# Performance work log

Hardware: AMD Instinct MI355X
Metric: run time of the kernel (lower is better)

Reference implementation:

```python
import jax, jax.numpy as jnp
import numpy as np

D_MODEL = 512
N_HEADS = 8
HEAD_SIZE = 64


def setup_inputs() -> dict:
    key = jax.random.key(0)
    ks = jax.random.split(key, 6)
    B, T = 4, 2048
    x_q = jax.random.normal(ks[0], (B, T, D_MODEL), dtype=jnp.float32)
    s = 1.0 / np.sqrt(D_MODEL)
    # per-head q/k/v projection weights, stacked: [H, head_size, d_model]
    Wq = jax.random.normal(ks[1], (N_HEADS, HEAD_SIZE, D_MODEL), dtype=jnp.float32) * s
    Wk = jax.random.normal(ks[2], (N_HEADS, HEAD_SIZE, D_MODEL), dtype=jnp.float32) * s
    Wv = jax.random.normal(ks[3], (N_HEADS, HEAD_SIZE, D_MODEL), dtype=jnp.float32) * s
    Wp = jax.random.normal(ks[4], (D_MODEL, D_MODEL), dtype=jnp.float32) * s
    bp = jax.random.normal(ks[5], (D_MODEL,), dtype=jnp.float32) * 0.01
    return {"x_q": x_q, "Wq": Wq, "Wk": Wk, "Wv": Wv, "Wp": Wp, "bp": bp}


def reference(x_q, Wq, Wk, Wv, Wp, bp):
    B, T, C = x_q.shape  # C == d_model
    # per-head projections: [B, H, T, K]
    q = jnp.einsum('btd,hkd->bhtk', x_q, Wq)
    k = jnp.einsum('btd,hkd->bhtk', x_q, Wk)
    v = jnp.einsum('btd,hkd->bhtk', x_q, Wv)
    # NOTE: original scales by C**-0.5 with C = d_model (not head_size)
    scores = jnp.einsum('bhtk,bhsk->bhts', q, k) * (C ** -0.5)
    causal = jnp.tril(jnp.ones((T, T), dtype=bool))
    scores = jnp.where(causal, scores, -jnp.inf)
    wei = jax.nn.softmax(scores, axis=-1)  # dropout is identity in eval
    out = jnp.einsum('bhts,bhsk->bhtk', wei, v)
    # concat heads: [B, T, H*K] == [B, T, d_model]
    out = out.transpose(0, 2, 1, 3).reshape(B, T, C)
    return out @ Wp.T + bp
```

## Files before the change

### kernel.cpp

```cpp
#include <hip/hip_runtime.h>
#include <hip/hip_bf16.h>

using bf16x8 = __attribute__((ext_vector_type(8))) __bf16;
using f32x4  = __attribute__((ext_vector_type(4))) float;
using f32x16 = __attribute__((ext_vector_type(16))) float;
using i32x4  = __attribute__((ext_vector_type(4))) int;

#define MFMA_16x16x32(a, b, c) __builtin_amdgcn_mfma_f32_16x16x32_bf16((a), (b), (c), 0, 0, 0)
#define MFMA32(a, b, c)        __builtin_amdgcn_mfma_f32_32x32x16_bf16((a), (b), (c), 0, 0, 0)

__device__ __forceinline__ ushort f2bf(float f) {
    return __builtin_bit_cast(ushort, (__bf16)f);
}
__device__ __forceinline__ unsigned pk_bf16(float lo, float hi) {
    unsigned r;
    asm volatile("v_cvt_pk_bf16_f32 %0, %1, %2" : "=v"(r) : "v"(lo), "v"(hi));
    return r;
}
__device__ __forceinline__ void pl32_swap(unsigned &a, unsigned &b) {
    asm volatile("v_permlane32_swap_b32 %0, %1" : "+v"(a), "+v"(b));
}

__global__ __launch_bounds__(256) void cvt_bf16(
    const float* __restrict__ in, ushort* __restrict__ out, int n)
{
    const int i = (blockIdx.x * 256 + threadIdx.x) * 8;
    if (i + 8 <= n) {
        const f32x4 a = *(const f32x4*)(in + i);
        const f32x4 b = *(const f32x4*)(in + i + 4);
        union { ushort u[8]; i32x4 w; } p;
        #pragma unroll
        for (int j = 0; j < 4; ++j) { p.u[j] = f2bf(a[j]); p.u[4 + j] = f2bf(b[j]); }
        *(i32x4*)(out + i) = p.w;
    }
}

__global__ __launch_bounds__(256) void gemm_qkv3(
    const ushort* __restrict__ A, const float* __restrict__ Wq,
    const float* __restrict__ Wk, const float* __restrict__ Wv,
    float qscale, ushort* __restrict__ qb, ushort* __restrict__ kb,
    ushort* __restrict__ vb)
{
    __shared__ ushort lA[128][40];
    __shared__ ushort lB[128][40];
    const int wsel = blockIdx.y >> 2;
    const int n0 = (blockIdx.y & 3) * 128;
    const float* W = (wsel == 0) ? Wq : ((wsel == 1) ? Wk : Wv);
    ushort* out = (wsel == 0) ? qb : ((wsel == 1) ? kb : vb);
    const float scale = (wsel == 0) ? qscale : 1.0f;

    const int m0 = blockIdx.x * 128;
    const int tid  = threadIdx.x;
    const int lane = tid & 63;
    const int wave = tid >> 6;
    const int wr = (wave >> 1) * 64, wc = (wave & 1) * 64;
    const int frow = lane & 15, fk = (lane >> 4) * 8;
    const int sr = tid >> 1, scc = (tid & 1) * 16;

    f32x4 acc[4][4] = {};

    for (int k0 = 0; k0 < 512; k0 += 32) {
        const ushort* pa = A + (m0 + sr) * 512 + k0 + scc;
        const i32x4 va0 = *(const i32x4*)(pa);
        const i32x4 va1 = *(const i32x4*)(pa + 8);
        const float* pb = W + (n0 + sr) * 512 + k0 + scc;
        const f32x4 b0 = *(const f32x4*)(pb);
        const f32x4 b1 = *(const f32x4*)(pb + 4);
        const f32x4 b2 = *(const f32x4*)(pb + 8);
        const f32x4 b3 = *(const f32x4*)(pb + 12);
        union { ushort u[16]; i32x4 w[2]; } pB;
        #pragma unroll
        for (int j = 0; j < 4; ++j) {
            pB.u[j]      = f2bf(b0[j]);  pB.u[4 + j]  = f2bf(b1[j]);
            pB.u[8 + j]  = f2bf(b2[j]);  pB.u[12 + j] = f2bf(b3[j]);
        }
        __syncthreads();
        *(i32x4*)&lA[sr][scc]     = va0;
        *(i32x4*)&lA[sr][scc + 8] = va1;
        *(i32x4*)&lB[sr][scc]     = pB.w[0];
        *(i32x4*)&lB[sr][scc + 8] = pB.w[1];
        __syncthreads();

        bf16x8 af[4], bg[4];
        #pragma unroll
        for (int m = 0; m < 4; ++m) af[m] = *(const bf16x8*)&lA[wr + m * 16 + frow][fk];
        #pragma unroll
        for (int n = 0; n < 4; ++n) bg[n] = *(const bf16x8*)&lB[wc + n * 16 + frow][fk];
        #pragma unroll
        for (int m = 0; m < 4; ++m)
            #pragma unroll
            for (int n = 0; n < 4; ++n)
                acc[m][n] = MFMA_16x16x32(af[m], bg[n], acc[m][n]);
    }

    const int rbase = (lane >> 4) * 4;
    const int ccol  = lane & 15;
    if (wsel == 2) {
        #pragma unroll
        for (int m = 0; m < 4; ++m)
            #pragma unroll
            for (int n = 0; n < 4; ++n) {
                const int col = n0 + wc + n * 16 + ccol;
                const int row0 = m0 + wr + m * 16 + rbase;
                unsigned long long u = 0;
                #pragma unroll
                for (int r = 0; r < 4; ++r)
                    u |= ((unsigned long long)f2bf(acc[m][n][r])) << (16 * r);
                const size_t idx = ((size_t)((row0 >> 11) * 8 + (col >> 6)) * 64
                                    + (col & 63)) * 2048 + (row0 & 2047);
                *(unsigned long long*)(out + idx) = u;
            }
    } else {
        #pragma unroll
        for (int m = 0; m < 4; ++m)
            #pragma unroll
            for (int n = 0; n < 4; ++n) {
                const int col = n0 + wc + n * 16 + ccol;
                #pragma unroll
                for (int r = 0; r < 4; ++r) {
                    const int row = m0 + wr + m * 16 + rbase + r;
                    out[(((row >> 11) * 8 + (col >> 6)) * 2048 + (row & 2047)) * 64 + (col & 63)]
                        = f2bf(acc[m][n][r] * scale);
                }
            }
    }
}

__global__ __launch_bounds__(256) void gemm_out(
    const ushort* __restrict__ A, const float* __restrict__ W,
    const float* __restrict__ bias, float* __restrict__ out)
{
    __shared__ ushort lA[128][40];
    __shared__ ushort lB[128][40];
    const int m0 = blockIdx.x * 128;
    const int n0 = blockIdx.y * 128;
    const int tid  = threadIdx.x;
    const int lane = tid & 63;
    const int wave = tid >> 6;
    const int wr = (wave >> 1) * 64, wc = (wave & 1) * 64;
    const int frow = lane & 15, fk = (lane >> 4) * 8;
    const int sr = tid >> 1, scc = (tid & 1) * 16;

    f32x4 acc[4][4] = {};

    for (int k0 = 0; k0 < 512; k0 += 32) {
        const int row = m0 + sr, c = k0 + scc;
        const ushort* pa = A + ((((row >> 11) * 8 + (c >> 6)) * 2048 + (row & 2047)) * 64 + (c & 63));
        const i32x4 va0 = *(const i32x4*)(pa);
        const i32x4 va1 = *(const i32x4*)(pa + 8);
        const float* pb = W + (n0 + sr) * 512 + k0 + scc;
        const f32x4 b0 = *(const f32x4*)(pb);
        const f32x4 b1 = *(const f32x4*)(pb + 4);
        const f32x4 b2 = *(const f32x4*)(pb + 8);
        const f32x4 b3 = *(const f32x4*)(pb + 12);
        union { ushort u[16]; i32x4 w[2]; } pB;
        #pragma unroll
        for (int j = 0; j < 4; ++j) {
            pB.u[j]      = f2bf(b0[j]);  pB.u[4 + j]  = f2bf(b1[j]);
            pB.u[8 + j]  = f2bf(b2[j]);  pB.u[12 + j] = f2bf(b3[j]);
        }
        __syncthreads();
        *(i32x4*)&lA[sr][scc]     = va0;
        *(i32x4*)&lA[sr][scc + 8] = va1;
        *(i32x4*)&lB[sr][scc]     = pB.w[0];
        *(i32x4*)&lB[sr][scc + 8] = pB.w[1];
        __syncthreads();

        bf16x8 af[4], bg[4];
        #pragma unroll
        for (int m = 0; m < 4; ++m) af[m] = *(const bf16x8*)&lA[wr + m * 16 + frow][fk];
        #pragma unroll
        for (int n = 0; n < 4; ++n) bg[n] = *(const bf16x8*)&lB[wc + n * 16 + frow][fk];
        #pragma unroll
        for (int m = 0; m < 4; ++m)
            #pragma unroll
            for (int n = 0; n < 4; ++n)
                acc[m][n] = MFMA_16x16x32(af[m], bg[n], acc[m][n]);
    }

    const int rbase = (lane >> 4) * 4;
    const int ccol  = lane & 15;
    #pragma unroll
    for (int m = 0; m < 4; ++m)
        #pragma unroll
        for (int n = 0; n < 4; ++n) {
            const int col = n0 + wc + n * 16 + ccol;
            const float bv = bias[col];
            #pragma unroll
            for (int r = 0; r < 4; ++r) {
                const int row = m0 + wr + m * 16 + rbase + r;
                out[row * 512 + col] = acc[m][n][r] + bv;
            }
        }
}

__global__ __launch_bounds__(256, 2) void attn_kernel(
    const ushort* __restrict__ q, const ushort* __restrict__ k,
    const ushort* __restrict__ vt, ushort* __restrict__ att)
{
    __shared__ ushort lK[2][64][64];
    __shared__ ushort lV[2][64][64];

    const int NB   = (int)(gridDim.x * gridDim.y);
    const int NH   = NB >> 4;
    const int half = NB >> 1;
    const int n    = (int)(blockIdx.y * gridDim.x + blockIdx.x);
    const int r    = (n < half) ? n : (NB - 1 - (n - half));
    const int qt0  = (15 - r / NH) * 128;
    const int bh   = r % NH;

    const ushort* Q  = q  + (size_t)bh * 2048 * 64;
    const ushort* K  = k  + (size_t)bh * 2048 * 64;
    const ushort* VT = vt + (size_t)bh * 2048 * 64;
    ushort* O = att + (size_t)bh * 2048 * 64;

    const int tid = threadIdx.x;
    const int wv  = tid >> 6;
    const int l   = tid & 63;
    const int ql  = l & 31;
    const int hi  = l >> 5;
    const int wrow0 = qt0 + wv * 32;
    const int qrow  = wrow0 + ql;
    const int wmax  = wrow0 + 31;
    const int qkey  = ql & 7;
    const float LOG2E = 1.44269504088896f;

    const int srow = tid >> 2;
    const int sg   = (tid & 3) * 2;
    const int skey = srow & 7;

    bf16x8 aq[4];
    #pragma unroll
    for (int kk = 0; kk < 4; ++kk)
        aq[kk] = *(const bf16x8*)(Q + (size_t)qrow * 64 + kk * 16 + hi * 8);

    f32x16 o0 = {}, o1 = {};
    float mrun = -30000.0f, lrun = 0.0f;
    const int nt = qt0 / 64 + 2;

    i32x4 kr0, kr1, vr0, vr1;
    auto loadG = [&](int s0) {
        const ushort* kp = K + (size_t)(s0 + srow) * 64 + (tid & 3) * 16;
        kr0 = *(const i32x4*)(kp);
        kr1 = *(const i32x4*)(kp + 8);
        const ushort* vp = VT + (size_t)srow * 2048 + s0 + (tid & 3) * 16;
        vr0 = *(const i32x4*)(vp);
        vr1 = *(const i32x4*)(vp + 8);
    };
    auto writeL = [&](int b) {
        *(i32x4*)&lK[b][srow][((sg    ) ^ skey) * 8] = kr0;
        *(i32x4*)&lK[b][srow][((sg + 1) ^ skey) * 8] = kr1;
        *(i32x4*)&lV[b][srow][((sg    ) ^ skey) * 8] = vr0;
        *(i32x4*)&lV[b][srow][((sg + 1) ^ skey) * 8] = vr1;
    };

    loadG(0);
    writeL(0);
    if (nt > 1) loadG(64);

    for (int t = 0; t < nt; ++t) {
        const int p  = t & 1;
        const int s0 = t * 64;
        __syncthreads();
        if (t + 1 < nt) writeL(p ^ 1);
        if (t + 2 < nt) loadG(s0 + 128);

        if (s0 > wmax) continue;

        f32x16 sa = {}, sb = {};
        #pragma unroll
        for (int kk = 0; kk < 4; ++kk) {
            const bf16x8 kb0 = *(const bf16x8*)&lK[p][ql]     [((2 * kk + hi) ^ qkey) * 8];
            const bf16x8 kb1 = *(const bf16x8*)&lK[p][32 + ql][((2 * kk + hi) ^ qkey) * 8];
            sa = MFMA32(kb0, aq[kk], sa);
            sb = MFMA32(kb1, aq[kk], sb);
        }

        if (s0 + 63 > wrow0) {
            #pragma unroll
            for (int rr = 0; rr < 16; ++rr) {
                const int cr = (rr & 3) + 8 * (rr >> 2) + 4 * hi;
                if (s0 + cr > qrow)      sa[rr] = -30000.0f;
                if (s0 + 32 + cr > qrow) sb[rr] = -30000.0f;
            }
        }

        float pmax = sa[0];
        #pragma unroll
        for (int rr = 1; rr < 16; ++rr) pmax = fmaxf(pmax, sa[rr]);
        #pragma unroll
        for (int rr = 0; rr < 16; ++rr) pmax = fmaxf(pmax, sb[rr]);
        pmax = fmaxf(pmax, __shfl_xor(pmax, 32));

        if (__any(pmax > mrun + 8.0f)) {
            const float mnew  = fmaxf(mrun, pmax);
            const float alpha = exp2f((mrun - mnew) * LOG2E);
            mrun = mnew;
            lrun *= alpha;
            #pragma unroll
            for (int rr = 0; rr < 16; ++rr) {
                const float ar = __shfl(alpha, (rr & 3) + 8 * (rr >> 2) + 4 * hi);
                o0[rr] *= ar; o1[rr] *= ar;
            }
        }

        const float mb = mrun * LOG2E;
        float ps = 0.0f;
        #pragma unroll
        for (int rr = 0; rr < 16; ++rr) {
            sa[rr] = exp2f(fmaf(sa[rr], LOG2E, -mb));
            sb[rr] = exp2f(fmaf(sb[rr], LOG2E, -mb));
            ps += sa[rr] + sb[rr];
        }
        ps += __shfl_xor(ps, 32);
        lrun += ps;

        unsigned paw[4][4];
        #pragma unroll
        for (int ks = 0; ks < 4; ++ks) {
            const int e = 2 * ks, f = 2 * ks + 1;
            const int ra = 4 * (e & 3), rb = 4 * (f & 3);
            unsigned A0, A1, B0, B1;
            if (e >> 2) { A0 = pk_bf16(sb[ra], sb[ra + 1]); A1 = pk_bf16(sb[ra + 2], sb[ra + 3]); }
            else        { A0 = pk_bf16(sa[ra], sa[ra + 1]); A1 = pk_bf16(sa[ra + 2], sa[ra + 3]); }
            if (f >> 2) { B0 = pk_bf16(sb[rb], sb[rb + 1]); B1 = pk_bf16(sb[rb + 2], sb[rb + 3]); }
            else        { B0 = pk_bf16(sa[rb], sa[rb + 1]); B1 = pk_bf16(sa[rb + 2], sa[rb + 3]); }
            pl32_swap(A0, B0);
            pl32_swap(A1, B1);
            paw[ks][0] = A0; paw[ks][1] = A1; paw[ks][2] = B0; paw[ks][3] = B1;
        }

        #pragma unroll
        for (int ks = 0; ks < 4; ++ks) {
            union { unsigned w[4]; bf16x8 v; } u;
            u.w[0] = paw[ks][0]; u.w[1] = paw[ks][1];
            u.w[2] = paw[ks][2]; u.w[3] = paw[ks][3];
            const bf16x8 v0 = *(const bf16x8*)&lV[p][ql]     [((2 * ks + hi) ^ qkey) * 8];
            const bf16x8 v1 = *(const bf16x8*)&lV[p][32 + ql][((2 * ks + hi) ^ qkey) * 8];
            o0 = MFMA32(u.v, v0, o0);
            o1 = MFMA32(u.v, v1, o1);
        }
    }

    const float linv = 1.0f / fmaxf(lrun, 1e-30f);
    #pragma unroll
    for (int rr = 0; rr < 16; ++rr) {
        const int cr = (rr & 3) + 8 * (rr >> 2) + 4 * hi;
        const float li = __shfl(linv, cr);
        const int row = wrow0 + cr;
        O[(size_t)row * 64 + ql]      = f2bf(o0[rr] * li);
        O[(size_t)row * 64 + 32 + ql] = f2bf(o1[rr] * li);
    }
}

extern "C" void kernel_launch(void* const* d_in, const int* in_sizes, int n_in,
                              void* d_out, int out_size, void* d_ws, size_t ws_size,
                              hipStream_t stream) {
    const float* x  = (const float*)d_in[0];
    const float* Wq = (const float*)d_in[1];
    const float* Wk = (const float*)d_in[2];
    const float* Wv = (const float*)d_in[3];
    const float* Wp = (const float*)d_in[4];
    const float* bp = (const float*)d_in[5];
    float* out = (float*)d_out;

    const size_t NEL  = 4u * 8u * 2048u * 64u;
    const size_t NELB = 8u * 2048u * 64u;
    const float qscale = 0.04419417382415922f;

    if (ws_size >= 3u * NEL * sizeof(ushort)) {
        ushort* xbf = (ushort*)d_out;
        ushort* qb  = xbf + NEL;
        ushort* kb  = (ushort*)d_ws;
        ushort* vb  = kb + NEL;
        ushort* ab  = vb + NEL;
        hipLaunchKernelGGL(cvt_bf16, dim3((int)(NEL / (256 * 8))), dim3(256), 0, stream,
                           x, xbf, (int)NEL);
        hipLaunchKernelGGL(gemm_qkv3, dim3(64, 12), dim3(256), 0, stream,
                           xbf, Wq, Wk, Wv, qscale, qb, kb, vb);
        hipLaunchKernelGGL(attn_kernel, dim3(16, 32), dim3(256), 0, stream, qb, kb, vb, ab);
        hipLaunchKernelGGL(gemm_out, dim3(64, 4), dim3(256), 0, stream, ab, Wp, bp, out);
    } else {
        ushort* kb = (ushort*)d_ws;
        ushort* vb = kb + NELB;
        ushort* ab = vb + NELB;
        for (int b = 0; b < 4; ++b) {
            const float* xb = x + (size_t)b * 2048u * 512u;
            float* ob = out + (size_t)b * 2048u * 512u;
            ushort* xbf = (ushort*)ob;
            ushort* qb  = xbf + NELB;
            hipLaunchKernelGGL(cvt_bf16, dim3((int)(NELB / (256 * 8))), dim3(256), 0, stream,
                               xb, xbf, (int)NELB);
            hipLaunchKernelGGL(gemm_qkv3, dim3(16, 12), dim3(256), 0, stream,
                               xbf, Wq, Wk, Wv, qscale, qb, kb, vb);
            hipLaunchKernelGGL(attn_kernel, dim3(16, 8), dim3(256), 0, stream, qb, kb, vb, ab);
            hipLaunchKernelGGL(gemm_out, dim3(16, 4), dim3(256), 0, stream, ab, Wp, bp, ob);
        }
    }
}
```

Baseline: 109.9 us.

## Pre-convert QKV weights to bf16 and halve attention query tile to 64 rows

Adds a kernel that converts Wq/Wk/Wv to bf16 once into the workspace (reusing the attention output buffer), so the QKV GEMM loads bf16 weights directly instead of converting fp32 in every tile. The attention kernel moves from 256 threads and 128-row query tiles to 128 threads and 64-row tiles, doubling the grid. The K/V staging is re-indexed so each thread loads four 16-byte chunks. This aims for more blocks and better causal load balance, at the cost of one extra launch and more K/V tile reloads per query row.

Result: slower. 119.8 us (+9.0%).

```diff
diff --git a/kernel.cpp b/kernel.cpp
--- a/kernel.cpp
+++ b/kernel.cpp
@@ -35,9 +35,23 @@
     }
 }
 
+__global__ __launch_bounds__(256) void cvt_w3(
+    const float* __restrict__ w0, const float* __restrict__ w1,
+    const float* __restrict__ w2, ushort* __restrict__ out)
+{
+    const int i = (blockIdx.x * 256 + threadIdx.x) * 8;
+    const int w = i >> 18, off = i & 262143;
+    const float* src = (w == 0) ? w0 : ((w == 1) ? w1 : w2);
+    const f32x4 a = *(const f32x4*)(src + off);
+    const f32x4 b = *(const f32x4*)(src + off + 4);
+    union { ushort u[8]; i32x4 v; } p;
+    #pragma unroll
+    for (int j = 0; j < 4; ++j) { p.u[j] = f2bf(a[j]); p.u[4 + j] = f2bf(b[j]); }
+    *(i32x4*)(out + i) = p.v;
+}
+
 __global__ __launch_bounds__(256) void gemm_qkv3(
-    const ushort* __restrict__ A, const float* __restrict__ Wq,
-    const float* __restrict__ Wk, const float* __restrict__ Wv,
+    const ushort* __restrict__ A, const ushort* __restrict__ Wbf,
     float qscale, ushort* __restrict__ qb, ushort* __restrict__ kb,
     ushort* __restrict__ vb)
 {
@@ -45,7 +59,7 @@
     __shared__ ushort lB[128][40];
     const int wsel = blockIdx.y >> 2;
     const int n0 = (blockIdx.y & 3) * 128;
-    const float* W = (wsel == 0) ? Wq : ((wsel == 1) ? Wk : Wv);
+    const ushort* W = Wbf + wsel * 262144;
     ushort* out = (wsel == 0) ? qb : ((wsel == 1) ? kb : vb);
     const float scale = (wsel == 0) ? qscale : 1.0f;
 
@@ -63,22 +77,14 @@
         const ushort* pa = A + (m0 + sr) * 512 + k0 + scc;
         const i32x4 va0 = *(const i32x4*)(pa);
         const i32x4 va1 = *(const i32x4*)(pa + 8);
-        const float* pb = W + (n0 + sr) * 512 + k0 + scc;
-        const f32x4 b0 = *(const f32x4*)(pb);
-        const f32x4 b1 = *(const f32x4*)(pb + 4);
-        const f32x4 b2 = *(const f32x4*)(pb + 8);
-        const f32x4 b3 = *(const f32x4*)(pb + 12);
-        union { ushort u[16]; i32x4 w[2]; } pB;
-        #pragma unroll
-        for (int j = 0; j < 4; ++j) {
-            pB.u[j]      = f2bf(b0[j]);  pB.u[4 + j]  = f2bf(b1[j]);
-            pB.u[8 + j]  = f2bf(b2[j]);  pB.u[12 + j] = f2bf(b3[j]);
-        }
+        const ushort* pb = W + (n0 + sr) * 512 + k0 + scc;
+        const i32x4 vb0 = *(const i32x4*)(pb);
+        const i32x4 vb1 = *(const i32x4*)(pb + 8);
         __syncthreads();
         *(i32x4*)&lA[sr][scc]     = va0;
         *(i32x4*)&lA[sr][scc + 8] = va1;
-        *(i32x4*)&lB[sr][scc]     = pB.w[0];
-        *(i32x4*)&lB[sr][scc + 8] = pB.w[1];
+        *(i32x4*)&lB[sr][scc]     = vb0;
+        *(i32x4*)&lB[sr][scc + 8] = vb1;
         __syncthreads();
 
         bf16x8 af[4], bg[4];
@@ -194,7 +200,7 @@
         }
 }
 
-__global__ __launch_bounds__(256, 2) void attn_kernel(
+__global__ __launch_bounds__(128) void attn_kernel(
     const ushort* __restrict__ q, const ushort* __restrict__ k,
     const ushort* __restrict__ vt, ushort* __restrict__ att)
 {
@@ -202,11 +208,11 @@
     __shared__ ushort lV[2][64][64];
 
     const int NB   = (int)(gridDim.x * gridDim.y);
-    const int NH   = NB >> 4;
+    const int NH   = (int)gridDim.y;
     const int half = NB >> 1;
     const int n    = (int)(blockIdx.y * gridDim.x + blockIdx.x);
     const int r    = (n < half) ? n : (NB - 1 - (n - half));
-    const int qt0  = (15 - r / NH) * 128;
+    const int qt0  = ((int)gridDim.x - 1 - r / NH) * 64;
     const int bh   = r % NH;
 
     const ushort* Q  = q  + (size_t)bh * 2048 * 64;
@@ -225,8 +231,8 @@
     const int qkey  = ql & 7;
     const float LOG2E = 1.44269504088896f;
 
-    const int srow = tid >> 2;
-    const int sg   = (tid & 3) * 2;
+    const int srow = tid >> 1;
+    const int sg   = (tid & 1) * 4;
     const int skey = srow & 7;
 
     bf16x8 aq[4];
@@ -236,22 +242,24 @@
 
     f32x16 o0 = {}, o1 = {};
     float mrun = -30000.0f, lrun = 0.0f;
-    const int nt = qt0 / 64 + 2;
-
-    i32x4 kr0, kr1, vr0, vr1;
+    const int nt = qt0 / 64 + 1;
+
+    i32x4 kr[4], vr[4];
     auto loadG = [&](int s0) {
-        const ushort* kp = K + (size_t)(s0 + srow) * 64 + (tid & 3) * 16;
-        kr0 = *(const i32x4*)(kp);
-        kr1 = *(const i32x4*)(kp + 8);
-        const ushort* vp = VT + (size_t)srow * 2048 + s0 + (tid & 3) * 16;
-        vr0 = *(const i32x4*)(vp);
-        vr1 = *(const i32x4*)(vp + 8);
+        const ushort* kp = K + (size_t)(s0 + srow) * 64 + sg * 8;
+        const ushort* vp = VT + (size_t)srow * 2048 + s0 + sg * 8;
+        #pragma unroll
+        for (int j = 0; j < 4; ++j) {
+            kr[j] = *(const i32x4*)(kp + j * 8);
+            vr[j] = *(const i32x4*)(vp + j * 8);
+        }
     };
     auto writeL = [&](int b) {
-        *(i32x4*)&lK[b][srow][((sg    ) ^ skey) * 8] = kr0;
-        *(i32x4*)&lK[b][srow][((sg + 1) ^ skey) * 8] = kr1;
-        *(i32x4*)&lV[b][srow][((sg    ) ^ skey) * 8] = vr0;
-        *(i32x4*)&lV[b][srow][((sg + 1) ^ skey) * 8] = vr1;
+        #pragma unroll
+        for (int j = 0; j < 4; ++j) {
+            *(i32x4*)&lK[b][srow][((sg + j) ^ skey) * 8] = kr[j];
+            *(i32x4*)&lV[b][srow][((sg + j) ^ skey) * 8] = vr[j];
+        }
     };
 
     loadG(0);
@@ -374,16 +382,19 @@
         ushort* kb  = (ushort*)d_ws;
         ushort* vb  = kb + NEL;
         ushort* ab  = vb + NEL;
+        ushort* wbf = ab;
         hipLaunchKernelGGL(cvt_bf16, dim3((int)(NEL / (256 * 8))), dim3(256), 0, stream,
                            x, xbf, (int)NEL);
+        hipLaunchKernelGGL(cvt_w3, dim3(384), dim3(256), 0, stream, Wq, Wk, Wv, wbf);
         hipLaunchKernelGGL(gemm_qkv3, dim3(64, 12), dim3(256), 0, stream,
-                           xbf, Wq, Wk, Wv, qscale, qb, kb, vb);
-        hipLaunchKernelGGL(attn_kernel, dim3(16, 32), dim3(256), 0, stream, qb, kb, vb, ab);
+                           xbf, wbf, qscale, qb, kb, vb);
+        hipLaunchKernelGGL(attn_kernel, dim3(32, 32), dim3(128), 0, stream, qb, kb, vb, ab);
         hipLaunchKernelGGL(gemm_out, dim3(64, 4), dim3(256), 0, stream, ab, Wp, bp, out);
     } else {
         ushort* kb = (ushort*)d_ws;
         ushort* vb = kb + NELB;
         ushort* ab = vb + NELB;
+        ushort* wbf = ab;
         for (int b = 0; b < 4; ++b) {
             const float* xb = x + (size_t)b * 2048u * 512u;
             float* ob = out + (size_t)b * 2048u * 512u;
@@ -391,9 +402,10 @@
             ushort* qb  = xbf + NELB;
             hipLaunchKernelGGL(cvt_bf16, dim3((int)(NELB / (256 * 8))), dim3(256), 0, stream,
                                xb, xbf, (int)NELB);
+            hipLaunchKernelGGL(cvt_w3, dim3(384), dim3(256), 0, stream, Wq, Wk, Wv, wbf);
             hipLaunchKernelGGL(gemm_qkv3, dim3(16, 12), dim3(256), 0, stream,
-                               xbf, Wq, Wk, Wv, qscale, qb, kb, vb);
-            hipLaunchKernelGGL(attn_kernel, dim3(16, 8), dim3(256), 0, stream, qb, kb, vb, ab);
+                               xbf, wbf, qscale, qb, kb, vb);
+            hipLaunchKernelGGL(attn_kernel, dim3(32, 8), dim3(128), 0, stream, qb, kb, vb, ab);
             hipLaunchKernelGGL(gemm_out, dim3(16, 4), dim3(256), 0, stream, ab, Wp, bp, ob);
         }
     }
```
